# Kernel optimization log

Hardware: AMD Instinct MI355X
Metric: run time of the kernel (lower is better)

Reference implementation:

```python
import jax, jax.numpy as jnp
import numpy as np

B, L, K, D, S = 8, 1024, 1024, 128, 16  # batch, nodes, eigvecs, d_model(=d_inner), d_state
ABAR_EPS = 1e-3
BN_EPS = 1e-5


def setup_inputs() -> dict:
    key = jax.random.key(0)
    ks = jax.random.split(key, 10)
    x = jax.random.normal(ks[0], (B, L, D), jnp.float32)
    attn_mask = jnp.ones((B, L), jnp.bool_)
    EigVecs = jax.random.normal(ks[1], (B, L, K), jnp.float32)
    EigVals = jax.random.uniform(ks[2], (B, K), jnp.float32)
    # BatchNorm1d (eval mode) params
    bn_gamma = jnp.ones((D,), jnp.float32)
    bn_beta = jnp.zeros((D,), jnp.float32)
    bn_mean = jnp.zeros((D,), jnp.float32)
    bn_var = jnp.ones((D,), jnp.float32)
    # in_proj Linear(D, 2*D)
    W_in = jax.random.normal(ks[3], (D, 2 * D), jnp.float32) / np.float32(np.sqrt(D))
    b_in = jnp.zeros((2 * D,), jnp.float32)
    # SSM params
    log_Delta = np.float32(np.log(1e-3)) + np.float32(np.log(0.1) - np.log(1e-3)) * jax.random.uniform(ks[4], (1, D), jnp.float32)
    Bp = 0.01 * jax.random.normal(ks[5], (1, D, S), jnp.float32)
    Cp = 0.01 * jax.random.normal(ks[6], (1, D, S), jnp.float32)
    log_A_real = jnp.log(0.5 * jnp.ones((D, S), jnp.float32))
    A_imag = jnp.pi * jnp.broadcast_to(jnp.arange(D, dtype=jnp.float32)[:, None], (D, S))
    # out_proj Linear(D, D)
    W_out = jax.random.normal(ks[7], (D, D), jnp.float32) / np.float32(np.sqrt(D))
    b_out = jnp.zeros((D,), jnp.float32)
    return {
        "x": x, "attn_mask": attn_mask, "EigVecs": EigVecs, "EigVals": EigVals,
        "bn_gamma": bn_gamma, "bn_beta": bn_beta, "bn_mean": bn_mean, "bn_var": bn_var,
        "W_in": W_in, "b_in": b_in, "log_Delta": log_Delta, "Bp": Bp, "Cp": Cp,
        "log_A_real": log_A_real, "A_imag": A_imag, "W_out": W_out, "b_out": b_out,
    }


def reference(x, attn_mask, EigVecs, EigVals, bn_gamma, bn_beta, bn_mean, bn_var,
              W_in, b_in, log_Delta, Bp, Cp, log_A_real, A_imag, W_out, b_out):
    # --- eig preprocessing ---
    ev = 1.0 - EigVals[:, :, None, None]            # (B,K,1,1)
    ev = jnp.nan_to_num(ev)
    Q = jnp.nan_to_num(EigVecs)                      # (B,L,K)
    Q = Q / jnp.linalg.norm(Q, axis=-1, keepdims=True)
    Q = jnp.nan_to_num(Q)
    # --- in_proj: BatchNorm1d (eval) + Linear ---
    xb = (x - bn_mean) * (bn_gamma / jnp.sqrt(bn_var + BN_EPS)) + bn_beta
    h = xb @ W_in + b_in                             # (B,L,2D)
    x1, z = jnp.split(h, 2, axis=-1)                 # split [d_model, d_model]
    u = x1 * jax.nn.silu(z)                          # (B,L,D)
    # --- discretized SSM params ---
    delta = jnp.exp(log_Delta)                       # (1,D)
    A = -jnp.exp(log_A_real) + 1j * A_imag           # (D,S) complex
    Abar = jnp.exp(-ABAR_EPS + delta[..., None] * A) # (1,D,S) complex
    Bbar = delta[..., None] * Bp                     # (1,D,S)
    # --- graph Fourier transform ---
    QTX = jnp.einsum('blk,bld->bkd', Q, u)           # (B,K,D)
    QTXB = QTX[..., None] * Bbar                     # (B,K,D,S)
    lamA = ev * Abar[:, None]                        # (B,K,D,S) complex
    lamQ = jnp.real(lamA / (1.0 - lamA) * QTXB)      # A_complex & not BC_complex -> .real
    # --- inverse transform + C reduction (fused) ---
    yssm = jnp.einsum('blk,bkds,ds->bld', Q, lamQ, Cp[0])  # (B,L,D)
    y = jax.nn.silu(yssm) @ W_out + b_out
    return y
```

## Files before the change

### kernel.cpp

```cpp
#include <hip/hip_runtime.h>
#include <math.h>

#define B_ 8
#define L_ 1024
#define K_ 1024
#define D_ 128
#define S_ 16
#define DS_ (D_ * S_)
#define NIT_ 16

typedef short bf16x8 __attribute__((ext_vector_type(8)));
typedef float f32x4 __attribute__((ext_vector_type(4)));
typedef __attribute__((address_space(1))) const unsigned int gu32;
typedef __attribute__((address_space(3))) unsigned int lu32;

__device__ inline unsigned short f2bf(float f) {
    unsigned int u = __float_as_uint(f);
    u = (u + 0x7fffu + ((u >> 16) & 1u)) >> 16;
    return (unsigned short)u;
}
__device__ inline float bf2f(unsigned short h) {
    return __uint_as_float(((unsigned int)h) << 16);
}

__device__ inline size_t bswz(int b, int c, int n) {
    return ((((size_t)b * 32 + (c >> 5)) * 4 + ((c >> 3) & 3)) * 128 + n) * 8;
}

__global__ __launch_bounds__(256) void k_pre(
    const float* __restrict__ E, const float* __restrict__ x,
    const float* __restrict__ g, const float* __restrict__ beta,
    const float* __restrict__ mean, const float* __restrict__ var,
    const float* __restrict__ W_in, const float* __restrict__ b_in,
    const float* __restrict__ log_Delta, const float* __restrict__ Bp,
    const float* __restrict__ Cp, const float* __restrict__ log_A_real,
    const float* __restrict__ A_imag,
    float* __restrict__ rn_out, float* __restrict__ par,
    unsigned short* __restrict__ uswH, unsigned short* __restrict__ uswL) {
    __shared__ float xb[16][128];
    __shared__ float rsum[16];
    __shared__ float rnS[16];
    int bx = blockIdx.x;
    int row0 = bx * 16;
    int t = threadIdx.x;
    if (bx < 8) {
        int i = bx * 256 + t;
        int d = i >> 4, s = i & 15;
        double delta = exp((double)log_Delta[d]);
        double Are = -exp((double)log_A_real[i]);
        double Aim = (double)A_imag[i];
        double mag = exp(-1e-3 + delta * Are);
        double ang = delta * Aim;
        int o = s * D_ + d;
        par[o]           = (float)(mag * cos(ang));
        par[DS_ + o]     = (float)(mag * sin(ang));
        par[2 * DS_ + o] = (float)(delta * (double)Bp[i] * (double)Cp[i]);
    }
    {
        int r = t >> 4, tt = t & 15;
        const float4* Ep = (const float4*)(E + (size_t)(row0 + r) * K_);
        float s = 0.f;
        #pragma unroll
        for (int i = 0; i < 16; ++i) {
            float4 v = Ep[tt + i * 16];
            s += v.x * v.x + v.y * v.y + v.z * v.z + v.w * v.w;
        }
        s += __shfl_xor(s, 8, 64);
        s += __shfl_xor(s, 4, 64);
        s += __shfl_xor(s, 2, 64);
        s += __shfl_xor(s, 1, 64);
        if (tt == 0) rsum[r] = s;
    }
    #pragma unroll
    for (int p = 0; p < 8; ++p) {
        int idx = t + p * 256;
        int dd = idx & 127, r = idx >> 7;
        float sc = g[dd] / sqrtf(var[dd] + 1e-5f);
        xb[r][dd] = (x[(size_t)(row0 + r) * D_ + dd] - mean[dd]) * sc + beta[dd];
    }
    __syncthreads();
    if (t < 16) {
        float rv = 1.0f / sqrtf(rsum[t]);
        rnS[t] = rv;
        rn_out[row0 + t] = rv;
    }
    __syncthreads();
    int j = t & 127, half = t >> 7;
    float acc1[8], acc2[8];
    #pragma unroll
    for (int r = 0; r < 8; ++r) { acc1[r] = 0.f; acc2[r] = 0.f; }
    #pragma unroll 4
    for (int dd = 0; dd < 128; ++dd) {
        float w1 = W_in[dd * 256 + j];
        float w2 = W_in[dd * 256 + 128 + j];
        #pragma unroll
        for (int r = 0; r < 8; ++r) {
            float xv = xb[half * 8 + r][dd];
            acc1[r] = fmaf(xv, w1, acc1[r]);
            acc2[r] = fmaf(xv, w2, acc2[r]);
        }
    }
    float b1 = b_in[j], b2 = b_in[128 + j];
    bf16x8 hv, lv;
    #pragma unroll
    for (int r = 0; r < 8; ++r) {
        int rr = half * 8 + r;
        float x1 = acc1[r] + b1;
        float z  = acc2[r] + b2;
        float sig = 1.0f / (1.0f + __expf(-z));
        float uv = rnS[rr] * x1 * z * sig;
        unsigned short h = f2bf(uv);
        hv[r] = (short)h;
        lv[r] = (short)f2bf(uv - bf2f(h));
    }
    int b = row0 >> 10;
    int l0 = (row0 & 1023) + half * 8;
    size_t off = bswz(b, l0, j);
    *(bf16x8*)&uswH[off] = hv;
    *(bf16x8*)&uswL[off] = lv;
}

#define STAGE_B(itS, nb)                                                        \
    _Pragma("unroll")                                                           \
    for (int j2 = 0; j2 < 4; ++j2) {                                            \
        int s = wave * 4 + j2;                         \
        int cts = s >> 4, s2 = s & 15;                                          \
        int qq = s2 & 3, nh = (s2 >> 2) & 1, hl = s2 >> 3;                      \
        size_t src0 = (size_t)((itS) * 2 + cts) * 4096;                         \
        const unsigned short* src =                                             \
            (hl ? BbL : BbH) + src0 + ((size_t)qq * 128 + nh * 64 + lane) * 8;  \
        unsigned short* dst =                                                   \
            (hl ? &sBl[nb][cts][0] : &sBh[nb][cts][0]) + qq * 1032 + nh * 512;  \
        __builtin_amdgcn_global_load_lds((gu32*)src, (lu32*)dst, 16, 0, 0);     \
    }

#define G1_WRITE_A(nb, v0, v1, v2, v3)                                           \
    {                                                                            \
        unsigned short h0 = f2bf(v0), h1 = f2bf(v1);                             \
        unsigned short l0 = f2bf((v0) - bf2f(h0)), l1 = f2bf((v1) - bf2f(h1));   \
        *(unsigned int*)&sAh[nb][0][aoff] = (unsigned)h0 | ((unsigned)h1 << 16); \
        *(unsigned int*)&sAl[nb][0][aoff] = (unsigned)l0 | ((unsigned)l1 << 16); \
        unsigned short h2 = f2bf(v2), h3 = f2bf(v3);                             \
        unsigned short l2 = f2bf((v2) - bf2f(h2)), l3 = f2bf((v3) - bf2f(h3));   \
        *(unsigned int*)&sAh[nb][1][aoff] = (unsigned)h2 | ((unsigned)h3 << 16); \
        *(unsigned int*)&sAl[nb][1][aoff] = (unsigned)l2 | ((unsigned)l3 << 16); \
    }

#define MFMA_PHASE(aB, cB)                                                       \
    {                                                                            \
        __builtin_amdgcn_s_setprio(1);                                           \
        bf16x8 ah[2], al[2], bh[2], bl[2];                                       \
        _Pragma("unroll")                                                        \
        for (int mt = 0; mt < 2; ++mt) {                                         \
            int row = mt * 16 + fr;                                              \
            int p = (q + (row >> 3)) & 3;                                        \
            int offA = row * 40 + p * 8;                                         \
            ah[mt] = *(const bf16x8*)&sAh[aB][kh][offA];                         \
            al[mt] = *(const bf16x8*)&sAl[aB][kh][offA];                         \
        }                                                                        \
        _Pragma("unroll")                                                        \
        for (int nt = 0; nt < 2; ++nt) {                                         \
            int offB = q * 1032 + (wn + nt * 16 + fr) * 8;                       \
            bh[nt] = *(const bf16x8*)&sBh[cB][kh][offB];                         \
            bl[nt] = *(const bf16x8*)&sBl[cB][kh][offB];                         \
        }                                                                        \
        _Pragma("unroll")                                                        \
        for (int mt = 0; mt < 2; ++mt)                                           \
            _Pragma("unroll")                                                    \
            for (int nt = 0; nt < 2; ++nt) {                                     \
                acc[mt][nt] = __builtin_amdgcn_mfma_f32_16x16x32_bf16(ah[mt], bh[nt], acc[mt][nt], 0, 0, 0); \
                acc[mt][nt] = __builtin_amdgcn_mfma_f32_16x16x32_bf16(ah[mt], bl[nt], acc[mt][nt], 0, 0, 0); \
                acc[mt][nt] = __builtin_amdgcn_mfma_f32_16x16x32_bf16(al[mt], bh[nt], acc[mt][nt], 0, 0, 0); \
            }                                                                    \
        __builtin_amdgcn_s_setprio(0);                                           \
    }

__global__ __launch_bounds__(512, 2) void k_g1(
    const float* __restrict__ E,
    const unsigned short* __restrict__ BH, const unsigned short* __restrict__ BL,
    const float* __restrict__ EigVals, const float* __restrict__ par,
    unsigned short* __restrict__ GswH, unsigned short* __restrict__ GswL) {
    __shared__ alignas(16) unsigned short sAh[2][2][1280], sAl[2][2][1280];
    __shared__ alignas(16) unsigned short sBh[3][2][4128], sBl[3][2][4128];
    __shared__ float evS[32];
    int bx = blockIdx.x;
    int b = bx & 7;
    int m0 = (bx >> 3) * 32;
    const float* Ab = E + (size_t)b * (1024 * 1024);
    const unsigned short* BbH = BH + (size_t)b * 131072;
    const unsigned short* BbL = BL + (size_t)b * 131072;
    int t = threadIdx.x;
    int wave = t >> 6, lane = t & 63;
    int fr = lane & 15, q = lane >> 4;
    int kh = wave & 1;
    int wn = (wave >> 1) * 32;
    int am = t & 31, jj = t >> 5;
    int ag = jj >> 2;
    int arot = (ag + (am >> 3)) & 3;
    int aoff = am * 40 + arot * 8 + ((2 * jj) & 7);
    if (t < 32) evS[t] = 1.0f - EigVals[b * 1024 + m0 + t];
    f32x4 acc[2][2];
    #pragma unroll
    for (int mt = 0; mt < 2; ++mt)
        #pragma unroll
        for (int nt = 0; nt < 2; ++nt)
            acc[mt][nt] = (f32x4){0.f, 0.f, 0.f, 0.f};

    {
        STAGE_B(0, 0);
        STAGE_B(1, 1);
        float v0 = Ab[(size_t)(2 * jj) * 1024 + m0 + am];
        float v1 = Ab[(size_t)(2 * jj + 1) * 1024 + m0 + am];
        float v2 = Ab[(size_t)(32 + 2 * jj) * 1024 + m0 + am];
        float v3 = Ab[(size_t)(32 + 2 * jj + 1) * 1024 + m0 + am];
        G1_WRITE_A(0, v0, v1, v2, v3);
        asm volatile("s_waitcnt vmcnt(0) lgkmcnt(0)" ::: "memory");
        __builtin_amdgcn_s_barrier();
        asm volatile("" ::: "memory");
    }

    for (int it = 0; it < NIT_; ++it) {
        int cB = it % 3;
        int fB = (it + 2) % 3;
        int aB = it & 1, naB = aB ^ 1;
        float v0 = 0.f, v1 = 0.f, v2 = 0.f, v3 = 0.f;
        if (it + 1 < NIT_) {
            int cb = (it + 1) * 64;
            v0 = Ab[(size_t)(cb + 2 * jj) * 1024 + m0 + am];
            v1 = Ab[(size_t)(cb + 2 * jj + 1) * 1024 + m0 + am];
            v2 = Ab[(size_t)(cb + 32 + 2 * jj) * 1024 + m0 + am];
            v3 = Ab[(size_t)(cb + 32 + 2 * jj + 1) * 1024 + m0 + am];
        }
        if (it + 2 < NIT_) STAGE_B(it + 2, fB);
        MFMA_PHASE(aB, cB)
        if (it + 1 < NIT_) G1_WRITE_A(naB, v0, v1, v2, v3);
        asm volatile("s_waitcnt lgkmcnt(0)" ::: "memory");
        __builtin_amdgcn_s_barrier();
        asm volatile("" ::: "memory");
    }

    float (*Gs)[132] = (float (*)[132])(&sBh[0][0][0]);
    if (kh == 0) {
        #pragma unroll
        for (int mt = 0; mt < 2; ++mt)
            #pragma unroll
            for (int nt = 0; nt < 2; ++nt) {
                int col = wn + nt * 16 + fr;
                #pragma unroll
                for (int r = 0; r < 4; ++r)
                    Gs[mt * 16 + q * 4 + r][col] = acc[mt][nt][r];
            }
    }
    __syncthreads();
    if (kh == 1) {
        #pragma unroll
        for (int mt = 0; mt < 2; ++mt)
            #pragma unroll
            for (int nt = 0; nt < 2; ++nt) {
                int col = wn + nt * 16 + fr;
                #pragma unroll
                for (int r = 0; r < 4; ++r)
                    Gs[mt * 16 + q * 4 + r][col] += acc[mt][nt][r];
            }
    }
    __syncthreads();
    {
        int col = t & 127, rowg = t >> 7;
        float arr[S_], aii[S_], ccc[S_];
        #pragma unroll
        for (int ss = 0; ss < S_; ++ss) {
            arr[ss] = par[ss * D_ + col];
            aii[ss] = par[DS_ + ss * D_ + col];
            ccc[ss] = par[2 * DS_ + ss * D_ + col];
        }
        #pragma unroll
        for (int i = 0; i < 8; ++i) {
            int row = rowg * 8 + i;
            float ev = evS[row];
            float w = 0.f;
            #pragma unroll
            for (int ss = 0; ss < S_; ++ss) {
                float a = ev * arr[ss], bi = ev * aii[ss];
                float oma = 1.0f - a;
                float b2 = bi * bi;
                float num = fmaf(a, oma, -b2);
                float den = fmaf(oma, oma, b2);
                float rr = __builtin_amdgcn_rcpf(den);
                rr = rr * (2.0f - den * rr);
                w = fmaf(ccc[ss], num * rr, w);
            }
            Gs[row][col] *= w;
        }
    }
    __syncthreads();
    {
        int d = t & 127, kg = t >> 7;
        bf16x8 hv, lv;
        #pragma unroll
        for (int i = 0; i < 8; ++i) {
            float v = Gs[kg * 8 + i][d];
            unsigned short h = f2bf(v);
            hv[i] = (short)h;
            lv[i] = (short)f2bf(v - bf2f(h));
        }
        int ct = m0 >> 5;
        size_t off = (((size_t)(b * 32 + ct) * 4 + kg) * 128 + d) * 8;
        *(bf16x8*)&GswH[off] = hv;
        *(bf16x8*)&GswL[off] = lv;
    }
}

#define G2_WRITE_A(nb, va)                                                       \
    {                                                                            \
        unsigned short h0 = f2bf((va).x), h1 = f2bf((va).y);                     \
        unsigned short h2 = f2bf((va).z), h3 = f2bf((va).w);                     \
        unsigned short l0 = f2bf((va).x - bf2f(h0)), l1 = f2bf((va).y - bf2f(h1));\
        unsigned short l2 = f2bf((va).z - bf2f(h2)), l3 = f2bf((va).w - bf2f(h3));\
        *(uint2*)&sAh[nb][chunk][aoff] =                                         \
            (uint2){(unsigned)h0 | ((unsigned)h1 << 16),                         \
                    (unsigned)h2 | ((unsigned)h3 << 16)};                        \
        *(uint2*)&sAl[nb][chunk][aoff] =                                         \
            (uint2){(unsigned)l0 | ((unsigned)l1 << 16),                         \
                    (unsigned)l2 | ((unsigned)l3 << 16)};                        \
    }

__global__ __launch_bounds__(512, 2) void k_g2(
    const float* __restrict__ E,
    const unsigned short* __restrict__ BH, const unsigned short* __restrict__ BL,
    const float* __restrict__ rn, const float* __restrict__ W_out,
    const float* __restrict__ b_out, float* __restrict__ y) {
    __shared__ alignas(16) unsigned short sAh[2][2][1280], sAl[2][2][1280];
    __shared__ alignas(16) unsigned short sBh[3][2][4128], sBl[3][2][4128];
    __shared__ float rnS[32];
    int bx = blockIdx.x;
    int b = bx & 7;
    int m0 = (bx >> 3) * 32;
    const float* Ab = E + (size_t)b * (1024 * 1024);
    const unsigned short* BbH = BH + (size_t)b * 131072;
    const unsigned short* BbL = BL + (size_t)b * 131072;
    int t = threadIdx.x;
    int wave = t >> 6, lane = t & 63;
    int fr = lane & 15, q = lane >> 4;
    int kh = wave & 1;
    int wn = (wave >> 1) * 32;
    int am = t >> 4, c4 = (t & 15) * 4;
    int chunk = c4 >> 5, cw = c4 & 31;
    int ag = cw >> 3;
    int arot = (ag + (am >> 3)) & 3;
    int aoff = am * 40 + arot * 8 + (cw & 7);
    if (t < 32) rnS[t] = rn[b * 1024 + m0 + t];
    f32x4 acc[2][2];
    #pragma unroll
    for (int mt = 0; mt < 2; ++mt)
        #pragma unroll
        for (int nt = 0; nt < 2; ++nt)
            acc[mt][nt] = (f32x4){0.f, 0.f, 0.f, 0.f};

    {
        STAGE_B(0, 0);
        STAGE_B(1, 1);
        float4 va = *(const float4*)&Ab[(size_t)(m0 + am) * 1024 + c4];
        G2_WRITE_A(0, va);
        asm volatile("s_waitcnt vmcnt(0) lgkmcnt(0)" ::: "memory");
        __builtin_amdgcn_s_barrier();
        asm volatile("" ::: "memory");
    }

    for (int it = 0; it < NIT_; ++it) {
        int cB = it % 3;
        int fB = (it + 2) % 3;
        int aB = it & 1, naB = aB ^ 1;
        float4 va = (float4){0.f, 0.f, 0.f, 0.f};
        if (it + 1 < NIT_)
            va = *(const float4*)&Ab[(size_t)(m0 + am) * 1024 + (it + 1) * 64 + c4];
        if (it + 2 < NIT_) STAGE_B(it + 2, fB);
        MFMA_PHASE(aB, cB)
        if (it + 1 < NIT_) G2_WRITE_A(naB, va);
        asm volatile("s_waitcnt lgkmcnt(0)" ::: "memory");
        __builtin_amdgcn_s_barrier();
        asm volatile("" ::: "memory");
    }

    float (*Ys)[132] = (float (*)[132])(&sBh[0][0][0]);
    if (kh == 0) {
        #pragma unroll
        for (int mt = 0; mt < 2; ++mt)
            #pragma unroll
            for (int nt = 0; nt < 2; ++nt) {
                int col = wn + nt * 16 + fr;
                #pragma unroll
                for (int r = 0; r < 4; ++r)
                    Ys[mt * 16 + q * 4 + r][col] = acc[mt][nt][r];
            }
    }
    __syncthreads();
    if (kh == 1) {
        #pragma unroll
        for (int mt = 0; mt < 2; ++mt)
            #pragma unroll
            for (int nt = 0; nt < 2; ++nt) {
                int col = wn + nt * 16 + fr;
                #pragma unroll
                for (int r = 0; r < 4; ++r)
                    Ys[mt * 16 + q * 4 + r][col] += acc[mt][nt][r];
            }
    }
    __syncthreads();
    {
        int col = t & 127, rowg = t >> 7;
        #pragma unroll
        for (int i = 0; i < 8; ++i) {
            int row = rowg * 8 + i;
            float v = Ys[row][col] * rnS[row];
            float sig = 1.0f / (1.0f + __expf(-v));
            Ys[row][col] = v * sig;
        }
    }
    __syncthreads();
    int j = t & 127, h = t >> 7;
    float a2[8];
    #pragma unroll
    for (int r = 0; r < 8; ++r) a2[r] = 0.f;
    for (int dd = 0; dd < 128; dd += 4) {
        float w0 = W_out[(dd + 0) * 128 + j];
        float w1 = W_out[(dd + 1) * 128 + j];
        float w2 = W_out[(dd + 2) * 128 + j];
        float w3 = W_out[(dd + 3) * 128 + j];
        #pragma unroll
        for (int r = 0; r < 8; ++r) {
            float4 yv = *(float4*)&Ys[h * 8 + r][dd];
            a2[r] = fmaf(yv.x, w0, a2[r]);
            a2[r] = fmaf(yv.y, w1, a2[r]);
            a2[r] = fmaf(yv.z, w2, a2[r]);
            a2[r] = fmaf(yv.w, w3, a2[r]);
        }
    }
    float bo = b_out[j];
    #pragma unroll
    for (int r = 0; r < 8; ++r)
        y[((size_t)b * 1024 + m0 + h * 8 + r) * 128 + j] = a2[r] + bo;
}

extern "C" void kernel_launch(void* const* d_in, const int* in_sizes, int n_in,
                              void* d_out, int out_size, void* d_ws, size_t ws_size,
                              hipStream_t stream) {
    const float* x          = (const float*)d_in[0];
    const float* EigVecs    = (const float*)d_in[2];
    const float* EigVals    = (const float*)d_in[3];
    const float* bn_gamma   = (const float*)d_in[4];
    const float* bn_beta    = (const float*)d_in[5];
    const float* bn_mean    = (const float*)d_in[6];
    const float* bn_var     = (const float*)d_in[7];
    const float* W_in       = (const float*)d_in[8];
    const float* b_in       = (const float*)d_in[9];
    const float* log_Delta  = (const float*)d_in[10];
    const float* Bp         = (const float*)d_in[11];
    const float* Cp         = (const float*)d_in[12];
    const float* log_A_real = (const float*)d_in[13];
    const float* A_imag     = (const float*)d_in[14];
    const float* W_out      = (const float*)d_in[15];
    const float* b_out      = (const float*)d_in[16];

    float* y = (float*)d_out;
    char* w = (char*)d_ws;
    float* rn            = (float*)(w);
    float* par           = (float*)(w + 32768);
    unsigned short* uswH = (unsigned short*)(w + 65536);
    unsigned short* uswL = (unsigned short*)(w + 65536 + (1u << 21));
    unsigned short* GswH = (unsigned short*)(w + 65536 + 2 * (1u << 21));
    unsigned short* GswL = (unsigned short*)(w + 65536 + 3 * (1u << 21));

    k_pre<<<dim3(B_ * L_ / 16), dim3(256), 0, stream>>>(
        EigVecs, x, bn_gamma, bn_beta, bn_mean, bn_var, W_in, b_in,
        log_Delta, Bp, Cp, log_A_real, A_imag, rn, par, uswH, uswL);
    k_g1<<<dim3(256), dim3(512), 0, stream>>>(
        EigVecs, uswH, uswL, EigVals, par, GswH, GswL);
    k_g2<<<dim3(256), dim3(512), 0, stream>>>(
        EigVecs, GswH, GswL, rn, W_out, b_out, y);
}
```

Baseline: 163.5 us.

## Compute in_proj GEMM in k_pre with split-bf16 MFMA instead of scalar FMAs

Replaces the scalar fp32 FMA loop for the BatchNorm+Linear in_proj in the preprocessing kernel with bf16 MFMA 16x16x32. Accuracy is kept close to fp32 by splitting activations and weights into high and low bf16 parts and issuing three MFMAs per tile. The SiLU gate and the x1 product are exchanged between waves through shared memory. Weights are converted to hi/lo bf16 per block on the fly, which adds conversion ALU work, extra LDS traffic and barriers.

```diff
diff --git a/kernel.cpp b/kernel.cpp
--- a/kernel.cpp
+++ b/kernel.cpp
@@ -37,7 +37,9 @@
     const float* __restrict__ A_imag,
     float* __restrict__ rn_out, float* __restrict__ par,
     unsigned short* __restrict__ uswH, unsigned short* __restrict__ uswL) {
-    __shared__ float xb[16][128];
+    __shared__ unsigned short xbh[4][16][32], xbl[4][16][32];
+    __shared__ float szs[16][132];
+    __shared__ float us[16][132];
     __shared__ float rsum[16];
     __shared__ float rnS[16];
     int bx = blockIdx.x;
@@ -76,7 +78,10 @@
         int idx = t + p * 256;
         int dd = idx & 127, r = idx >> 7;
         float sc = g[dd] / sqrtf(var[dd] + 1e-5f);
-        xb[r][dd] = (x[(size_t)(row0 + r) * D_ + dd] - mean[dd]) * sc + beta[dd];
+        float v = (x[(size_t)(row0 + r) * D_ + dd] - mean[dd]) * sc + beta[dd];
+        unsigned short h = f2bf(v);
+        xbh[dd >> 5][r][dd & 31] = h;
+        xbl[dd >> 5][r][dd & 31] = f2bf(v - bf2f(h));
     }
     __syncthreads();
     if (t < 16) {
@@ -85,30 +90,64 @@
         rn_out[row0 + t] = rv;
     }
     __syncthreads();
+    int wave = t >> 6, lane = t & 63;
+    int fr = lane & 15, q = lane >> 4;
+    f32x4 acc[4];
+    #pragma unroll
+    for (int ct = 0; ct < 4; ++ct) acc[ct] = (f32x4){0.f, 0.f, 0.f, 0.f};
+    #pragma unroll
+    for (int c = 0; c < 4; ++c) {
+        bf16x8 ah = *(const bf16x8*)&xbh[c][fr][q * 8];
+        bf16x8 al = *(const bf16x8*)&xbl[c][fr][q * 8];
+        #pragma unroll
+        for (int ct = 0; ct < 4; ++ct) {
+            int col = wave * 64 + ct * 16 + fr;
+            bf16x8 bh, bl;
+            #pragma unroll
+            for (int i = 0; i < 8; ++i) {
+                float wv = W_in[(c * 32 + q * 8 + i) * 256 + col];
+                unsigned short h = f2bf(wv);
+                bh[i] = (short)h;
+                bl[i] = (short)f2bf(wv - bf2f(h));
+            }
+            acc[ct] = __builtin_amdgcn_mfma_f32_16x16x32_bf16(ah, bh, acc[ct], 0, 0, 0);
+            acc[ct] = __builtin_amdgcn_mfma_f32_16x16x32_bf16(ah, bl, acc[ct], 0, 0, 0);
+            acc[ct] = __builtin_amdgcn_mfma_f32_16x16x32_bf16(al, bh, acc[ct], 0, 0, 0);
+        }
+    }
+    if (wave >= 2) {
+        #pragma unroll
+        for (int ct = 0; ct < 4; ++ct) {
+            int cz = (wave - 2) * 64 + ct * 16 + fr;
+            float b2v = b_in[128 + cz];
+            #pragma unroll
+            for (int r = 0; r < 4; ++r) {
+                float z = acc[ct][r] + b2v;
+                float sig = 1.0f / (1.0f + __expf(-z));
+                szs[q * 4 + r][cz] = z * sig;
+            }
+        }
+    }
+    __syncthreads();
+    if (wave < 2) {
+        #pragma unroll
+        for (int ct = 0; ct < 4; ++ct) {
+            int cx = wave * 64 + ct * 16 + fr;
+            float b1v = b_in[cx];
+            #pragma unroll
+            for (int r = 0; r < 4; ++r) {
+                int row = q * 4 + r;
+                float x1 = acc[ct][r] + b1v;
+                us[row][cx] = rnS[row] * x1 * szs[row][cx];
+            }
+        }
+    }
+    __syncthreads();
     int j = t & 127, half = t >> 7;
-    float acc1[8], acc2[8];
-    #pragma unroll
-    for (int r = 0; r < 8; ++r) { acc1[r] = 0.f; acc2[r] = 0.f; }
-    #pragma unroll 4
-    for (int dd = 0; dd < 128; ++dd) {
-        float w1 = W_in[dd * 256 + j];
-        float w2 = W_in[dd * 256 + 128 + j];
-        #pragma unroll
-        for (int r = 0; r < 8; ++r) {
-            float xv = xb[half * 8 + r][dd];
-            acc1[r] = fmaf(xv, w1, acc1[r]);
-            acc2[r] = fmaf(xv, w2, acc2[r]);
-        }
-    }
-    float b1 = b_in[j], b2 = b_in[128 + j];
     bf16x8 hv, lv;
     #pragma unroll
     for (int r = 0; r < 8; ++r) {
-        int rr = half * 8 + r;
-        float x1 = acc1[r] + b1;
-        float z  = acc2[r] + b2;
-        float sig = 1.0f / (1.0f + __expf(-z));
-        float uv = rnS[rr] * x1 * z * sig;
+        float uv = us[half * 8 + r][j];
         unsigned short h = f2bf(uv);
         hv[r] = (short)h;
         lv[r] = (short)f2bf(uv - bf2f(h));
```

Result: faster. 159.5 us (-2.4%).
